# Optimization experiments

Measured on AMD Instinct MI355X. Metric: run time of the kernel, lower is better.

The kernel has to match this reference:

```python
import jax, jax.numpy as jnp
import numpy as np

N_NODES = 100000
N_EDGES = 1600000
D = 128  # feat_input_size_node == embed_inside_size == feat_target_size


def gcn_layer(x, W, b, row, col, ew, n_nodes):
    """PyG GCNConv with scalar edge_weight, add_self_loops=True, normalize=True.
    x: [N, Fin], W: [Fout, Fin], b: [Fout], row/col: [E], ew: [E].
    Messages flow row -> col (source_to_target)."""
    h = x @ W.T  # [N, Fout]
    # degree includes self-loop weight 1.0 per node
    deg = jax.ops.segment_sum(ew, col, num_segments=n_nodes) + 1.0  # [N]
    dinv = jnp.where(deg > 0, jax.lax.rsqrt(deg), 0.0)  # [N]
    norm = dinv[row] * ew * dinv[col]  # [E]
    msgs = norm[:, None] * h[row]  # [E, Fout] -- gather
    agg = jax.ops.segment_sum(msgs, col, num_segments=n_nodes)  # scatter-add
    agg = agg + (dinv * dinv)[:, None] * h  # self-loop contribution (weight 1)
    return agg + b


def setup_inputs() -> dict:
    key = jax.random.key(0)
    k1, k2, k3, k4, k5, k6, k7 = jax.random.split(key, 7)
    edge_tuples = jax.random.randint(k1, (2, N_EDGES), 0, N_NODES, dtype=jnp.int64) if jax.config.jax_enable_x64 else jax.random.randint(k1, (2, N_EDGES), 0, N_NODES).astype(jnp.int32)
    edge_feats = jax.random.uniform(k2, (N_EDGES, 1), dtype=jnp.float32)
    node_feats = jax.random.normal(k3, (N_NODES, D), dtype=jnp.float32)
    s1 = 1.0 / np.sqrt(D)
    W1 = jax.random.uniform(k4, (D, D), minval=-s1, maxval=s1, dtype=jnp.float32)
    b1 = jnp.zeros((D,), dtype=jnp.float32)
    W2 = jax.random.uniform(k5, (D, D), minval=-s1, maxval=s1, dtype=jnp.float32)
    b2 = jnp.zeros((D,), dtype=jnp.float32)
    return {"edge_tuples": edge_tuples, "edge_feats": edge_feats, "node_feats": node_feats,
            "W1": W1, "b1": b1, "W2": W2, "b2": b2}


def reference(edge_tuples, edge_feats, node_feats, W1, b1, W2, b2):
    row, col = edge_tuples[0], edge_tuples[1]
    ew = edge_feats.squeeze(-1)  # [E]
    n = node_feats.shape[0]
    h = gcn_layer(node_feats, W1, b1, row, col, ew, n)
    h = jnp.tanh(h)  # activate='tanh' between the two GCN layers
    out = gcn_layer(h, W2, b2, row, col, ew, n)
    # skip=Identity (Fin==Fout), doskip=1
    return out + node_feats
```

## Files before the change

### kernel.cpp

```cpp
#include <hip/hip_runtime.h>
#include <math.h>

#define D 128
#define EPB 4096
#define MAXNB 800

typedef unsigned long long ull;
typedef unsigned short ushort_t;
typedef __attribute__((ext_vector_type(8))) short bf16x8;
typedef __attribute__((ext_vector_type(4))) float f32x4;

__device__ __forceinline__ float bf_lo(unsigned u) { return __uint_as_float(u << 16); }
__device__ __forceinline__ float bf_hi(unsigned u) { return __uint_as_float(u & 0xffff0000u); }
__device__ __forceinline__ unsigned bpack(float a, float b) {
  unsigned ua = __float_as_uint(a), ub = __float_as_uint(b);
  ua += 0x7fff + ((ua >> 16) & 1);
  ub += 0x7fff + ((ub >> 16) & 1);
  return (ua >> 16) | (ub & 0xffff0000u);
}
__device__ __forceinline__ ushort_t bh16(float a) {
  unsigned ua = __float_as_uint(a);
  ua += 0x7fff + ((ua >> 16) & 1);
  return (ushort_t)(ua >> 16);
}

__global__ __launch_bounds__(256) void k_h1(const int* __restrict__ col, int E, int B1, int B1pad,
                                            int* __restrict__ gh, int NB,
                                            const float2* __restrict__ x2, unsigned* __restrict__ xb, int n64,
                                            const float* __restrict__ W1, const float* __restrict__ W2,
                                            ushort_t* __restrict__ Whi1, ushort_t* __restrict__ Wlo1,
                                            ushort_t* __restrict__ Whi2, ushort_t* __restrict__ Wlo2) {
  int b = blockIdx.x, t = threadIdx.x;
  if (b < B1) {
    __shared__ int h[MAXNB];
    for (int i = t; i < NB; i += 256) h[i] = 0;
    __syncthreads();
    int e0 = b * EPB, e1 = min(E, e0 + EPB);
    for (int e = e0 + t; e < e1; e += 256) atomicAdd(&h[col[e] >> 7], 1);
    __syncthreads();
    for (int i = t; i < NB; i += 256) gh[i * B1pad + b] = h[i];
    return;
  }
  int idx = (b - B1) * 256 + t;
  if (idx < n64) { float2 v = x2[idx]; xb[idx] = bpack(v.x, v.y); return; }
  int j = idx - n64;
  if (j >= 2 * D * D) return;
  const float* W = (j < D * D) ? W1 : W2;
  ushort_t* Hh = (j < D * D) ? Whi1 : Whi2;
  ushort_t* Hl = (j < D * D) ? Wlo1 : Wlo2;
  int k = j & (D * D - 1);
  float w = W[k];
  ushort_t hh = bh16(w);
  Hh[k] = hh;
  Hl[k] = bh16(w - __uint_as_float((unsigned)hh << 16));
}

__global__ __launch_bounds__(512) void k_hscan(int* __restrict__ gh, int* __restrict__ binTotal,
                                               int B1, int B1pad) {
  __shared__ int wsum[8];
  int bin = blockIdx.x, t = threadIdx.x;
  int v = (t < B1) ? gh[bin * B1pad + t] : 0;
  int lane = t & 63, wid = t >> 6;
  int x = v;
  #pragma unroll
  for (int d = 1; d < 64; d <<= 1) { int y = __shfl_up(x, d, 64); if (lane >= d) x += y; }
  if (lane == 63) wsum[wid] = x;
  __syncthreads();
  int woff = 0;
  for (int w = 0; w < wid; ++w) woff += wsum[w];
  if (t < B1) gh[bin * B1pad + t] = woff + x - v;
  if (t == 511) binTotal[bin] = woff + x;
}

__device__ __forceinline__ int block_excl_scan(int v, int t, int* wsum, int* total) {
  int lane = t & 63, wid = t >> 6;
  int x = v;
  #pragma unroll
  for (int d = 1; d < 64; d <<= 1) {
    int y = __shfl_up(x, d, 64);
    if (lane >= d) x += y;
  }
  if (lane == 63) wsum[wid] = x;
  __syncthreads();
  int woff = 0;
  for (int w = 0; w < wid; ++w) woff += wsum[w];
  if (total) { int tot = 0; for (int w = 0; w < 4; ++w) tot += wsum[w]; *total = tot; }
  return woff + x - v;
}

__global__ __launch_bounds__(256) void k_scatter(const int* __restrict__ row, const int* __restrict__ col,
                                                 const float* __restrict__ ew,
                                                 const int* __restrict__ gh, const int* __restrict__ binTotal,
                                                 int B1pad, int NB,
                                                 ull* __restrict__ a_e, int E) {
  __shared__ ull recs[EPB];
  __shared__ int hist[MAXNB];
  __shared__ int cur[MAXNB];
  __shared__ int wb[MAXNB];
  __shared__ int bbase[MAXNB];
  __shared__ int wsum[4];
  int b = blockIdx.x, t = threadIdx.x;
  for (int i = t; i < NB; i += 256) { hist[i] = 0; cur[i] = 0; }
  __syncthreads();
  int e0 = b * EPB;
  int cnt = min(E - e0, EPB);
  ull v[16];
  #pragma unroll
  for (int k = 0; k < 16; ++k) {
    int idx = t + k * 256;
    v[k] = 0;
    if (idx < cnt) {
      int e = e0 + idx;
      int c = col[e];
      unsigned q = __float2uint_rn(ew[e] * 32767.0f);
      if (q > 32767u) q = 32767u;
      unsigned hi = ((unsigned)c << 15) | q;
      v[k] = ((ull)hi << 32) | (unsigned)row[e];
      atomicAdd(&hist[hi >> 22], 1);
    }
  }
  __syncthreads();
  int base = t * 4;
  int bt[4]; int sb = 0;
  #pragma unroll
  for (int u = 0; u < 4; ++u) { bt[u] = (base + u < NB) ? binTotal[base + u] : 0; sb += bt[u]; }
  int exb = block_excl_scan(sb, t, wsum, nullptr);
  {
    int run = exb;
    #pragma unroll
    for (int u = 0; u < 4; ++u) { if (base + u < NB) bbase[base + u] = run; run += bt[u]; }
  }
  __syncthreads();
  int hv[4];
  #pragma unroll
  for (int u = 0; u < 4; ++u) hv[u] = (base + u < NB) ? hist[base + u] : 0;
  int s = hv[0] + hv[1] + hv[2] + hv[3];
  int excl = block_excl_scan(s, t, wsum, nullptr);
  int run = excl;
  #pragma unroll
  for (int u = 0; u < 4; ++u) {
    if (base + u < NB) {
      hist[base + u] = run;
      wb[base + u] = bbase[base + u] + gh[(base + u) * B1pad + b] - run;
    }
    run += hv[u];
  }
  __syncthreads();
  #pragma unroll
  for (int k = 0; k < 16; ++k) {
    if (t + k * 256 < cnt) {
      unsigned bkt = (unsigned)(v[k] >> 54);
      int idx = hist[bkt] + atomicAdd(&cur[bkt], 1);
      recs[idx] = v[k];
    }
  }
  __syncthreads();
  for (int i = t; i < cnt; i += 256) {
    ull r = recs[i];
    a_e[wb[(unsigned)(r >> 54)] + i] = r;
  }
}

__global__ __launch_bounds__(256) void k_bucket(const ull* __restrict__ a_e,
                                                const int* __restrict__ binTotal,
                                                int* __restrict__ offs, float* __restrict__ dinv,
                                                unsigned* __restrict__ sorted2, int N, int E, int NB) {
  __shared__ int hist[128];
  __shared__ float wdeg[128];
  __shared__ int pfx[128];
  __shared__ int cur[128];
  __shared__ int wred[4];
  __shared__ int s0sh;
  int bin = blockIdx.x, t = threadIdx.x;
  if (t < 128) { hist[t] = 0; wdeg[t] = 0.f; cur[t] = 0; }
  int part = 0;
  for (int j = t; j < NB; j += 256) if (j < bin) part += binTotal[j];
  #pragma unroll
  for (int d = 32; d >= 1; d >>= 1) part += __shfl_xor(part, d, 64);
  if ((t & 63) == 0) wred[t >> 6] = part;
  __syncthreads();
  if (t == 0) s0sh = wred[0] + wred[1] + wred[2] + wred[3];
  if (t == 0 && bin == 0) offs[N] = E;
  __syncthreads();
  int s0 = s0sh;
  int s1 = s0 + binTotal[bin];
  for (int i = s0 + t; i < s1; i += 256) {
    unsigned hi = (unsigned)(a_e[i] >> 32);
    int lc = (hi >> 15) & 127;
    atomicAdd(&hist[lc], 1);
    atomicAdd(&wdeg[lc], (float)(hi & 32767u) * (1.0f / 32767.0f));
  }
  __syncthreads();
  if (t == 0) { int run = 0; for (int i = 0; i < 128; ++i) { pfx[i] = run; run += hist[i]; } }
  __syncthreads();
  int c0 = bin << 7;
  if (t < 128 && c0 + t < N) {
    offs[c0 + t] = s0 + pfx[t];
    dinv[c0 + t] = rsqrtf(wdeg[t] + 1.0f);
  }
  for (int i = s0 + t; i < s1; i += 256) {
    ull v = a_e[i];
    unsigned hi = (unsigned)(v >> 32);
    int lc = (hi >> 15) & 127;
    int pos = s0 + pfx[lc] + atomicAdd(&cur[lc], 1);
    sorted2[pos] = ((unsigned)v << 15) | (hi & 32767u);
  }
}

__global__ __launch_bounds__(256) void k_agg(const unsigned* __restrict__ H2,
                                             const unsigned* __restrict__ elist,
                                             const int* __restrict__ offs, const float* __restrict__ dinv,
                                             unsigned* __restrict__ outb, int N) {
  int lane = threadIdx.x & 63;
  int c = blockIdx.x * 4 + (threadIdx.x >> 6);
  if (c >= N) return;
  int start = offs[c];
  int m = offs[c + 1] - start;
  int q = lane >> 4;
  int fi = lane & 15;
  float dv = dinv[c];
  float dcs = dv * (1.0f / 32767.0f);
  float a0 = 0.f, a1 = 0.f, a2 = 0.f, a3 = 0.f, a4 = 0.f, a5 = 0.f, a6 = 0.f, a7 = 0.f;
  for (int base = 0; base < m; base += 64) {
    int chunk = min(64, m - base);
    unsigned rec = (lane < chunk) ? elist[start + base + lane] : 0u;
    int iters = (chunk + 3) >> 2;
    int i = 0;
    for (; i + 4 <= iters; i += 4) {
      unsigned e0 = __shfl(rec, 4 * i + q, 64);
      unsigned e1 = __shfl(rec, 4 * i + 4 + q, 64);
      unsigned e2 = __shfl(rec, 4 * i + 8 + q, 64);
      unsigned e3 = __shfl(rec, 4 * i + 12 + q, 64);
      uint4 u0 = *(const uint4*)&H2[(size_t)(e0 >> 15) * 64 + fi * 4];
      uint4 u1 = *(const uint4*)&H2[(size_t)(e1 >> 15) * 64 + fi * 4];
      uint4 u2 = *(const uint4*)&H2[(size_t)(e2 >> 15) * 64 + fi * 4];
      uint4 u3 = *(const uint4*)&H2[(size_t)(e3 >> 15) * 64 + fi * 4];
      float w0 = (float)(e0 & 0x7fffu) * dinv[e0 >> 15] * dcs;
      float w1 = (float)(e1 & 0x7fffu) * dinv[e1 >> 15] * dcs;
      float w2 = (float)(e2 & 0x7fffu) * dinv[e2 >> 15] * dcs;
      float w3 = (float)(e3 & 0x7fffu) * dinv[e3 >> 15] * dcs;
      a0 += w0 * bf_lo(u0.x); a1 += w0 * bf_hi(u0.x);
      a2 += w0 * bf_lo(u0.y); a3 += w0 * bf_hi(u0.y);
      a4 += w0 * bf_lo(u0.z); a5 += w0 * bf_hi(u0.z);
      a6 += w0 * bf_lo(u0.w); a7 += w0 * bf_hi(u0.w);
      a0 += w1 * bf_lo(u1.x); a1 += w1 * bf_hi(u1.x);
      a2 += w1 * bf_lo(u1.y); a3 += w1 * bf_hi(u1.y);
      a4 += w1 * bf_lo(u1.z); a5 += w1 * bf_hi(u1.z);
      a6 += w1 * bf_lo(u1.w); a7 += w1 * bf_hi(u1.w);
      a0 += w2 * bf_lo(u2.x); a1 += w2 * bf_hi(u2.x);
      a2 += w2 * bf_lo(u2.y); a3 += w2 * bf_hi(u2.y);
      a4 += w2 * bf_lo(u2.z); a5 += w2 * bf_hi(u2.z);
      a6 += w2 * bf_lo(u2.w); a7 += w2 * bf_hi(u2.w);
      a0 += w3 * bf_lo(u3.x); a1 += w3 * bf_hi(u3.x);
      a2 += w3 * bf_lo(u3.y); a3 += w3 * bf_hi(u3.y);
      a4 += w3 * bf_lo(u3.z); a5 += w3 * bf_hi(u3.z);
      a6 += w3 * bf_lo(u3.w); a7 += w3 * bf_hi(u3.w);
    }
    for (; i < iters; ++i) {
      unsigned e0 = __shfl(rec, 4 * i + q, 64);
      float w0 = (float)(e0 & 0x7fffu) * dinv[e0 >> 15] * dcs;
      uint4 u0 = *(const uint4*)&H2[(size_t)(e0 >> 15) * 64 + fi * 4];
      a0 += w0 * bf_lo(u0.x); a1 += w0 * bf_hi(u0.x);
      a2 += w0 * bf_lo(u0.y); a3 += w0 * bf_hi(u0.y);
      a4 += w0 * bf_lo(u0.z); a5 += w0 * bf_hi(u0.z);
      a6 += w0 * bf_lo(u0.w); a7 += w0 * bf_hi(u0.w);
    }
  }
  a0 += __shfl_xor(a0, 16, 64); a0 += __shfl_xor(a0, 32, 64);
  a1 += __shfl_xor(a1, 16, 64); a1 += __shfl_xor(a1, 32, 64);
  a2 += __shfl_xor(a2, 16, 64); a2 += __shfl_xor(a2, 32, 64);
  a3 += __shfl_xor(a3, 16, 64); a3 += __shfl_xor(a3, 32, 64);
  a4 += __shfl_xor(a4, 16, 64); a4 += __shfl_xor(a4, 32, 64);
  a5 += __shfl_xor(a5, 16, 64); a5 += __shfl_xor(a5, 32, 64);
  a6 += __shfl_xor(a6, 16, 64); a6 += __shfl_xor(a6, 32, 64);
  a7 += __shfl_xor(a7, 16, 64); a7 += __shfl_xor(a7, 32, 64);
  if (q == 0) {
    float sw = dv * dv;
    uint4 us = *(const uint4*)&H2[(size_t)c * 64 + fi * 4];
    a0 += sw * bf_lo(us.x); a1 += sw * bf_hi(us.x);
    a2 += sw * bf_lo(us.y); a3 += sw * bf_hi(us.y);
    a4 += sw * bf_lo(us.z); a5 += sw * bf_hi(us.z);
    a6 += sw * bf_lo(us.w); a7 += sw * bf_hi(us.w);
    uint4 o;
    o.x = bpack(a0, a1); o.y = bpack(a2, a3); o.z = bpack(a4, a5); o.w = bpack(a6, a7);
    *(uint4*)&outb[(size_t)c * 64 + fi * 4] = o;
  }
}

template<int TANH, int SKIP>
__global__ __launch_bounds__(256) void k_mgemm(const ushort_t* __restrict__ S,
                                               const ushort_t* __restrict__ Whi,
                                               const ushort_t* __restrict__ Wlo,
                                               const float* __restrict__ bias,
                                               const ushort_t* __restrict__ skipb,
                                               void* __restrict__ outv, int n) {
  int wave = threadIdx.x >> 6, lane = threadIdx.x & 63;
  int cl = lane & 15;
  int kg = lane >> 4;
  int cb0 = wave * 2;

  bf16x8 bh[2][4], bl[2][4];
  float bv[2];
  #pragma unroll
  for (int c = 0; c < 2; ++c) {
    int col = (cb0 + c) * 16 + cl;
    const ushort_t* wh = Whi + (size_t)col * D + kg * 8;
    const ushort_t* wl = Wlo + (size_t)col * D + kg * 8;
    #pragma unroll
    for (int kt = 0; kt < 4; ++kt) {
      bh[c][kt] = *(const bf16x8*)(wh + kt * 32);
      bl[c][kt] = *(const bf16x8*)(wl + kt * 32);
    }
    bv[c] = bias[col];
  }

  int ntiles = (n + 15) >> 4;
  for (int t = blockIdx.x; t < ntiles; t += gridDim.x) {
    int arow = t * 16 + cl; if (arow >= n) arow = n - 1;
    const ushort_t* srow = S + (size_t)arow * D + kg * 8;
    bf16x8 a[4];
    #pragma unroll
    for (int kt = 0; kt < 4; ++kt) a[kt] = *(const bf16x8*)(srow + kt * 32);
    #pragma unroll
    for (int c = 0; c < 2; ++c) {
      f32x4 acc = {0.f, 0.f, 0.f, 0.f};
      #pragma unroll
      for (int kt = 0; kt < 4; ++kt)
        acc = __builtin_amdgcn_mfma_f32_16x16x32_bf16(a[kt], bh[c][kt], acc, 0, 0, 0);
      #pragma unroll
      for (int kt = 0; kt < 4; ++kt)
        acc = __builtin_amdgcn_mfma_f32_16x16x32_bf16(a[kt], bl[c][kt], acc, 0, 0, 0);
      int col = (cb0 + c) * 16 + cl;
      #pragma unroll
      for (int i = 0; i < 4; ++i) {
        int r = t * 16 + kg * 4 + i;
        if (r < n) {
          float o = acc[i] + bv[c];
          if (TANH) {
            o = tanhf(o);
            ((ushort_t*)outv)[(size_t)r * D + col] = bh16(o);
          } else {
            if (SKIP) o += __uint_as_float((unsigned)skipb[(size_t)r * D + col] << 16);
            ((float*)outv)[(size_t)r * D + col] = o;
          }
        }
      }
    }
  }
}

extern "C" void kernel_launch(void* const* d_in, const int* in_sizes, int n_in,
                              void* d_out, int out_size, void* d_ws, size_t ws_size,
                              hipStream_t stream) {
  const int*   et = (const int*)d_in[0];
  const float* ef = (const float*)d_in[1];
  const float* x  = (const float*)d_in[2];
  const float* W1 = (const float*)d_in[3];
  const float* b1 = (const float*)d_in[4];
  const float* W2 = (const float*)d_in[5];
  const float* b2 = (const float*)d_in[6];

  int E = in_sizes[1];
  int N = in_sizes[2] / D;
  const int* row = et;
  const int* col = et + E;

  int NB = (N + 127) >> 7;
  int B1 = (E + EPB - 1) / EPB;
  int B1pad = (B1 + 7) & ~7;

  char* p = (char*)d_ws;
  auto alloc = [&](size_t bytes) { char* q = p; p += (bytes + 255) & ~(size_t)255; return q; };
  int*      gh       = (int*)     alloc((size_t)NB * B1pad * 4);
  int*      binTotal = (int*)     alloc((size_t)NB * 4);
  ull*      a_e      = (ull*)     alloc((size_t)E * 8);
  unsigned* elist    = (unsigned*)alloc((size_t)E * 4);
  int*      offs     = (int*)     alloc((size_t)(N + 1) * 4);
  float*    dinv     = (float*)   alloc((size_t)N * 4);
  unsigned* xb       = (unsigned*)alloc((size_t)N * 64 * 4);
  unsigned* s2b      = (unsigned*)alloc((size_t)N * 64 * 4);
  ushort_t* whi1 = (ushort_t*)alloc(D * D * 2);
  ushort_t* wlo1 = (ushort_t*)alloc(D * D * 2);
  ushort_t* whi2 = (ushort_t*)alloc(D * D * 2);
  ushort_t* wlo2 = (ushort_t*)alloc(D * D * 2);
  unsigned* s1b = (unsigned*)d_out;
  unsigned* a1b = s1b + (size_t)N * 64;

  int prepBlocks = (N * 64 + 2 * D * D + 255) / 256;
  k_h1<<<B1 + prepBlocks, 256, 0, stream>>>(col, E, B1, B1pad, gh, NB,
                                            (const float2*)x, xb, N * 64,
                                            W1, W2, whi1, wlo1, whi2, wlo2);
  k_hscan<<<NB, 512, 0, stream>>>(gh, binTotal, B1, B1pad);
  k_scatter<<<B1, 256, 0, stream>>>(row, col, ef, gh, binTotal, B1pad, NB, a_e, E);
  k_bucket<<<NB, 256, 0, stream>>>(a_e, binTotal, offs, dinv, elist, N, E, NB);

  int ab = (N + 3) / 4;
  int gb = 1024;
  k_agg<<<ab, 256, 0, stream>>>(xb, elist, offs, dinv, s1b, N);
  k_mgemm<1, 0><<<gb, 256, 0, stream>>>((const ushort_t*)s1b, whi1, wlo1, b1, nullptr, a1b, N);
  k_agg<<<ab, 256, 0, stream>>>(a1b, elist, offs, dinv, s2b, N);
  k_mgemm<0, 1><<<gb, 256, 0, stream>>>((const ushort_t*)s2b, whi2, wlo2, b2,
                                        (const ushort_t*)xb, d_out, N);
}
```

Baseline: 240.0 us.

## Halve scatter block size and stage bucket sort through LDS

```diff
diff --git a/kernel.cpp b/kernel.cpp
--- a/kernel.cpp
+++ b/kernel.cpp
@@ -2,8 +2,9 @@
 #include <math.h>
 
 #define D 128
-#define EPB 4096
+#define EPB 2048
 #define MAXNB 800
+#define BCAP 3072
 
 typedef unsigned long long ull;
 typedef unsigned short ushort_t;
@@ -55,9 +56,9 @@
   Hl[k] = bh16(w - __uint_as_float((unsigned)hh << 16));
 }
 
-__global__ __launch_bounds__(512) void k_hscan(int* __restrict__ gh, int* __restrict__ binTotal,
-                                               int B1, int B1pad) {
-  __shared__ int wsum[8];
+__global__ __launch_bounds__(1024) void k_hscan(int* __restrict__ gh, int* __restrict__ binTotal,
+                                                int B1, int B1pad) {
+  __shared__ int wsum[16];
   int bin = blockIdx.x, t = threadIdx.x;
   int v = (t < B1) ? gh[bin * B1pad + t] : 0;
   int lane = t & 63, wid = t >> 6;
@@ -69,7 +70,7 @@
   int woff = 0;
   for (int w = 0; w < wid; ++w) woff += wsum[w];
   if (t < B1) gh[bin * B1pad + t] = woff + x - v;
-  if (t == 511) binTotal[bin] = woff + x;
+  if (t == 1023) binTotal[bin] = woff + x;
 }
 
 __device__ __forceinline__ int block_excl_scan(int v, int t, int* wsum, int* total) {
@@ -104,9 +105,9 @@
   __syncthreads();
   int e0 = b * EPB;
   int cnt = min(E - e0, EPB);
-  ull v[16];
-  #pragma unroll
-  for (int k = 0; k < 16; ++k) {
+  ull v[EPB / 256];
+  #pragma unroll
+  for (int k = 0; k < EPB / 256; ++k) {
     int idx = t + k * 256;
     v[k] = 0;
     if (idx < cnt) {
@@ -147,7 +148,7 @@
   }
   __syncthreads();
   #pragma unroll
-  for (int k = 0; k < 16; ++k) {
+  for (int k = 0; k < EPB / 256; ++k) {
     if (t + k * 256 < cnt) {
       unsigned bkt = (unsigned)(v[k] >> 54);
       int idx = hist[bkt] + atomicAdd(&cur[bkt], 1);
@@ -165,6 +166,8 @@
                                                 const int* __restrict__ binTotal,
                                                 int* __restrict__ offs, float* __restrict__ dinv,
                                                 unsigned* __restrict__ sorted2, int N, int E, int NB) {
+  __shared__ ull recLds[BCAP];
+  __shared__ unsigned sortLds[BCAP];
   __shared__ int hist[128];
   __shared__ float wdeg[128];
   __shared__ int pfx[128];
@@ -183,9 +186,14 @@
   if (t == 0 && bin == 0) offs[N] = E;
   __syncthreads();
   int s0 = s0sh;
-  int s1 = s0 + binTotal[bin];
-  for (int i = s0 + t; i < s1; i += 256) {
-    unsigned hi = (unsigned)(a_e[i] >> 32);
+  int cnt = binTotal[bin];
+  int fits = (cnt <= BCAP);
+  if (fits) {
+    for (int i = t; i < cnt; i += 256) recLds[i] = a_e[s0 + i];
+    __syncthreads();
+  }
+  for (int i = t; i < cnt; i += 256) {
+    unsigned hi = (unsigned)((fits ? recLds[i] : a_e[s0 + i]) >> 32);
     int lc = (hi >> 15) & 127;
     atomicAdd(&hist[lc], 1);
     atomicAdd(&wdeg[lc], (float)(hi & 32767u) * (1.0f / 32767.0f));
@@ -198,12 +206,17 @@
     offs[c0 + t] = s0 + pfx[t];
     dinv[c0 + t] = rsqrtf(wdeg[t] + 1.0f);
   }
-  for (int i = s0 + t; i < s1; i += 256) {
-    ull v = a_e[i];
+  for (int i = t; i < cnt; i += 256) {
+    ull v = fits ? recLds[i] : a_e[s0 + i];
     unsigned hi = (unsigned)(v >> 32);
     int lc = (hi >> 15) & 127;
-    int pos = s0 + pfx[lc] + atomicAdd(&cur[lc], 1);
-    sorted2[pos] = ((unsigned)v << 15) | (hi & 32767u);
+    int pos = pfx[lc] + atomicAdd(&cur[lc], 1);
+    unsigned sv = ((unsigned)v << 15) | (hi & 32767u);
+    if (fits) sortLds[pos] = sv; else sorted2[s0 + pos] = sv;
+  }
+  if (fits) {
+    __syncthreads();
+    for (int i = t; i < cnt; i += 256) sorted2[s0 + i] = sortLds[i];
   }
 }
 
@@ -390,7 +403,7 @@
   k_h1<<<B1 + prepBlocks, 256, 0, stream>>>(col, E, B1, B1pad, gh, NB,
                                             (const float2*)x, xb, N * 64,
                                             W1, W2, whi1, wlo1, whi2, wlo2);
-  k_hscan<<<NB, 512, 0, stream>>>(gh, binTotal, B1, B1pad);
+  k_hscan<<<NB, 1024, 0, stream>>>(gh, binTotal, B1, B1pad);
   k_scatter<<<B1, 256, 0, stream>>>(row, col, ef, gh, binTotal, B1pad, NB, a_e, E);
   k_bucket<<<NB, 256, 0, stream>>>(a_e, binTotal, offs, dinv, elist, N, E, NB);
 
```

Result: slower. 245.8 us (+2.4%).

## Fuse neighbor aggregation with the MFMA GEMM through an LDS row tile

Applied to the files above, without the earlier changes.

```diff
diff --git a/kernel.cpp b/kernel.cpp
--- a/kernel.cpp
+++ b/kernel.cpp
@@ -207,142 +207,132 @@
   }
 }
 
-__global__ __launch_bounds__(256) void k_agg(const unsigned* __restrict__ H2,
-                                             const unsigned* __restrict__ elist,
-                                             const int* __restrict__ offs, const float* __restrict__ dinv,
-                                             unsigned* __restrict__ outb, int N) {
-  int lane = threadIdx.x & 63;
-  int c = blockIdx.x * 4 + (threadIdx.x >> 6);
-  if (c >= N) return;
-  int start = offs[c];
-  int m = offs[c + 1] - start;
-  int q = lane >> 4;
-  int fi = lane & 15;
-  float dv = dinv[c];
-  float dcs = dv * (1.0f / 32767.0f);
-  float a0 = 0.f, a1 = 0.f, a2 = 0.f, a3 = 0.f, a4 = 0.f, a5 = 0.f, a6 = 0.f, a7 = 0.f;
-  for (int base = 0; base < m; base += 64) {
-    int chunk = min(64, m - base);
-    unsigned rec = (lane < chunk) ? elist[start + base + lane] : 0u;
-    int iters = (chunk + 3) >> 2;
-    int i = 0;
-    for (; i + 4 <= iters; i += 4) {
-      unsigned e0 = __shfl(rec, 4 * i + q, 64);
-      unsigned e1 = __shfl(rec, 4 * i + 4 + q, 64);
-      unsigned e2 = __shfl(rec, 4 * i + 8 + q, 64);
-      unsigned e3 = __shfl(rec, 4 * i + 12 + q, 64);
-      uint4 u0 = *(const uint4*)&H2[(size_t)(e0 >> 15) * 64 + fi * 4];
-      uint4 u1 = *(const uint4*)&H2[(size_t)(e1 >> 15) * 64 + fi * 4];
-      uint4 u2 = *(const uint4*)&H2[(size_t)(e2 >> 15) * 64 + fi * 4];
-      uint4 u3 = *(const uint4*)&H2[(size_t)(e3 >> 15) * 64 + fi * 4];
-      float w0 = (float)(e0 & 0x7fffu) * dinv[e0 >> 15] * dcs;
-      float w1 = (float)(e1 & 0x7fffu) * dinv[e1 >> 15] * dcs;
-      float w2 = (float)(e2 & 0x7fffu) * dinv[e2 >> 15] * dcs;
-      float w3 = (float)(e3 & 0x7fffu) * dinv[e3 >> 15] * dcs;
-      a0 += w0 * bf_lo(u0.x); a1 += w0 * bf_hi(u0.x);
-      a2 += w0 * bf_lo(u0.y); a3 += w0 * bf_hi(u0.y);
-      a4 += w0 * bf_lo(u0.z); a5 += w0 * bf_hi(u0.z);
-      a6 += w0 * bf_lo(u0.w); a7 += w0 * bf_hi(u0.w);
-      a0 += w1 * bf_lo(u1.x); a1 += w1 * bf_hi(u1.x);
-      a2 += w1 * bf_lo(u1.y); a3 += w1 * bf_hi(u1.y);
-      a4 += w1 * bf_lo(u1.z); a5 += w1 * bf_hi(u1.z);
-      a6 += w1 * bf_lo(u1.w); a7 += w1 * bf_hi(u1.w);
-      a0 += w2 * bf_lo(u2.x); a1 += w2 * bf_hi(u2.x);
-      a2 += w2 * bf_lo(u2.y); a3 += w2 * bf_hi(u2.y);
-      a4 += w2 * bf_lo(u2.z); a5 += w2 * bf_hi(u2.z);
-      a6 += w2 * bf_lo(u2.w); a7 += w2 * bf_hi(u2.w);
-      a0 += w3 * bf_lo(u3.x); a1 += w3 * bf_hi(u3.x);
-      a2 += w3 * bf_lo(u3.y); a3 += w3 * bf_hi(u3.y);
-      a4 += w3 * bf_lo(u3.z); a5 += w3 * bf_hi(u3.z);
-      a6 += w3 * bf_lo(u3.w); a7 += w3 * bf_hi(u3.w);
-    }
-    for (; i < iters; ++i) {
-      unsigned e0 = __shfl(rec, 4 * i + q, 64);
-      float w0 = (float)(e0 & 0x7fffu) * dinv[e0 >> 15] * dcs;
-      uint4 u0 = *(const uint4*)&H2[(size_t)(e0 >> 15) * 64 + fi * 4];
-      a0 += w0 * bf_lo(u0.x); a1 += w0 * bf_hi(u0.x);
-      a2 += w0 * bf_lo(u0.y); a3 += w0 * bf_hi(u0.y);
-      a4 += w0 * bf_lo(u0.z); a5 += w0 * bf_hi(u0.z);
-      a6 += w0 * bf_lo(u0.w); a7 += w0 * bf_hi(u0.w);
-    }
-  }
-  a0 += __shfl_xor(a0, 16, 64); a0 += __shfl_xor(a0, 32, 64);
-  a1 += __shfl_xor(a1, 16, 64); a1 += __shfl_xor(a1, 32, 64);
-  a2 += __shfl_xor(a2, 16, 64); a2 += __shfl_xor(a2, 32, 64);
-  a3 += __shfl_xor(a3, 16, 64); a3 += __shfl_xor(a3, 32, 64);
-  a4 += __shfl_xor(a4, 16, 64); a4 += __shfl_xor(a4, 32, 64);
-  a5 += __shfl_xor(a5, 16, 64); a5 += __shfl_xor(a5, 32, 64);
-  a6 += __shfl_xor(a6, 16, 64); a6 += __shfl_xor(a6, 32, 64);
-  a7 += __shfl_xor(a7, 16, 64); a7 += __shfl_xor(a7, 32, 64);
-  if (q == 0) {
-    float sw = dv * dv;
-    uint4 us = *(const uint4*)&H2[(size_t)c * 64 + fi * 4];
-    a0 += sw * bf_lo(us.x); a1 += sw * bf_hi(us.x);
-    a2 += sw * bf_lo(us.y); a3 += sw * bf_hi(us.y);
-    a4 += sw * bf_lo(us.z); a5 += sw * bf_hi(us.z);
-    a6 += sw * bf_lo(us.w); a7 += sw * bf_hi(us.w);
-    uint4 o;
-    o.x = bpack(a0, a1); o.y = bpack(a2, a3); o.z = bpack(a4, a5); o.w = bpack(a6, a7);
-    *(uint4*)&outb[(size_t)c * 64 + fi * 4] = o;
-  }
-}
-
 template<int TANH, int SKIP>
-__global__ __launch_bounds__(256) void k_mgemm(const ushort_t* __restrict__ S,
+__global__ __launch_bounds__(256) void k_aggmm(const unsigned* __restrict__ H2,
+                                               const unsigned* __restrict__ elist,
+                                               const int* __restrict__ offs, const float* __restrict__ dinv,
                                                const ushort_t* __restrict__ Whi,
                                                const ushort_t* __restrict__ Wlo,
                                                const float* __restrict__ bias,
                                                const ushort_t* __restrict__ skipb,
-                                               void* __restrict__ outv, int n) {
-  int wave = threadIdx.x >> 6, lane = threadIdx.x & 63;
-  int cl = lane & 15;
-  int kg = lane >> 4;
+                                               void* __restrict__ outv, int N) {
+  __shared__ ushort_t sRow[16][136];
+  int t = threadIdx.x;
+  int wave = t >> 6, lane = t & 63;
+  int q = lane >> 4;
+  int fi = lane & 15;
+  int blk = blockIdx.x;
+
+  for (int sub = 0; sub < 4; ++sub) {
+    int row = wave * 4 + sub;
+    int c = blk * 16 + row;
+    if (c < N) {
+      int start = offs[c];
+      int m = offs[c + 1] - start;
+      float dv = dinv[c];
+      float dcs = dv * (1.0f / 32767.0f);
+      float a0 = 0.f, a1 = 0.f, a2 = 0.f, a3 = 0.f, a4 = 0.f, a5 = 0.f, a6 = 0.f, a7 = 0.f;
+      for (int base = 0; base < m; base += 64) {
+        int chunk = min(64, m - base);
+        unsigned rec = (lane < chunk) ? elist[start + base + lane] : 0u;
+        int iters = (chunk + 3) >> 2;
+        int i = 0;
+        for (; i + 4 <= iters; i += 4) {
+          unsigned e0 = __shfl(rec, 4 * i + q, 64);
+          unsigned e1 = __shfl(rec, 4 * i + 4 + q, 64);
+          unsigned e2 = __shfl(rec, 4 * i + 8 + q, 64);
+          unsigned e3 = __shfl(rec, 4 * i + 12 + q, 64);
+          uint4 u0 = *(const uint4*)&H2[(size_t)(e0 >> 15) * 64 + fi * 4];
+          uint4 u1 = *(const uint4*)&H2[(size_t)(e1 >> 15) * 64 + fi * 4];
+          uint4 u2 = *(const uint4*)&H2[(size_t)(e2 >> 15) * 64 + fi * 4];
+          uint4 u3 = *(const uint4*)&H2[(size_t)(e3 >> 15) * 64 + fi * 4];
+          float w0 = (float)(e0 & 0x7fffu) * dinv[e0 >> 15] * dcs;
+          float w1 = (float)(e1 & 0x7fffu) * dinv[e1 >> 15] * dcs;
+          float w2 = (float)(e2 & 0x7fffu) * dinv[e2 >> 15] * dcs;
+          float w3 = (float)(e3 & 0x7fffu) * dinv[e3 >> 15] * dcs;
+          a0 += w0 * bf_lo(u0.x); a1 += w0 * bf_hi(u0.x);
+          a2 += w0 * bf_lo(u0.y); a3 += w0 * bf_hi(u0.y);
+          a4 += w0 * bf_lo(u0.z); a5 += w0 * bf_hi(u0.z);
+          a6 += w0 * bf_lo(u0.w); a7 += w0 * bf_hi(u0.w);
+          a0 += w1 * bf_lo(u1.x); a1 += w1 * bf_hi(u1.x);
+          a2 += w1 * bf_lo(u1.y); a3 += w1 * bf_hi(u1.y);
+          a4 += w1 * bf_lo(u1.z); a5 += w1 * bf_hi(u1.z);
+          a6 += w1 * bf_lo(u1.w); a7 += w1 * bf_hi(u1.w);
+          a0 += w2 * bf_lo(u2.x); a1 += w2 * bf_hi(u2.x);
+          a2 += w2 * bf_lo(u2.y); a3 += w2 * bf_hi(u2.y);
+          a4 += w2 * bf_lo(u2.z); a5 += w2 * bf_hi(u2.z);
+          a6 += w2 * bf_lo(u2.w); a7 += w2 * bf_hi(u2.w);
+          a0 += w3 * bf_lo(u3.x); a1 += w3 * bf_hi(u3.x);
+          a2 += w3 * bf_lo(u3.y); a3 += w3 * bf_hi(u3.y);
+          a4 += w3 * bf_lo(u3.z); a5 += w3 * bf_hi(u3.z);
+          a6 += w3 * bf_lo(u3.w); a7 += w3 * bf_hi(u3.w);
+        }
+        for (; i < iters; ++i) {
+          unsigned e0 = __shfl(rec, 4 * i + q, 64);
+          float w0 = (float)(e0 & 0x7fffu) * dinv[e0 >> 15] * dcs;
+          uint4 u0 = *(const uint4*)&H2[(size_t)(e0 >> 15) * 64 + fi * 4];
+          a0 += w0 * bf_lo(u0.x); a1 += w0 * bf_hi(u0.x);
+          a2 += w0 * bf_lo(u0.y); a3 += w0 * bf_hi(u0.y);
+          a4 += w0 * bf_lo(u0.z); a5 += w0 * bf_hi(u0.z);
+          a6 += w0 * bf_lo(u0.w); a7 += w0 * bf_hi(u0.w);
+        }
+      }
+      a0 += __shfl_xor(a0, 16, 64); a0 += __shfl_xor(a0, 32, 64);
+      a1 += __shfl_xor(a1, 16, 64); a1 += __shfl_xor(a1, 32, 64);
+      a2 += __shfl_xor(a2, 16, 64); a2 += __shfl_xor(a2, 32, 64);
+      a3 += __shfl_xor(a3, 16, 64); a3 += __shfl_xor(a3, 32, 64);
+      a4 += __shfl_xor(a4, 16, 64); a4 += __shfl_xor(a4, 32, 64);
+      a5 += __shfl_xor(a5, 16, 64); a5 += __shfl_xor(a5, 32, 64);
+      a6 += __shfl_xor(a6, 16, 64); a6 += __shfl_xor(a6, 32, 64);
+      a7 += __shfl_xor(a7, 16, 64); a7 += __shfl_xor(a7, 32, 64);
+      if (q == 0) {
+        float sw = dv * dv;
+        uint4 us = *(const uint4*)&H2[(size_t)c * 64 + fi * 4];
+        a0 += sw * bf_lo(us.x); a1 += sw * bf_hi(us.x);
+        a2 += sw * bf_lo(us.y); a3 += sw * bf_hi(us.y);
+        a4 += sw * bf_lo(us.z); a5 += sw * bf_hi(us.z);
+        a6 += sw * bf_lo(us.w); a7 += sw * bf_hi(us.w);
+        uint4 o;
+        o.x = bpack(a0, a1); o.y = bpack(a2, a3); o.z = bpack(a4, a5); o.w = bpack(a6, a7);
+        *(uint4*)&sRow[row][fi * 8] = o;
+      }
+    } else if (q == 0) {
+      uint4 z = make_uint4(0, 0, 0, 0);
+      *(uint4*)&sRow[row][fi * 8] = z;
+    }
+  }
+  __syncthreads();
+
+  int cl = fi;
+  int kg = q;
   int cb0 = wave * 2;
-
-  bf16x8 bh[2][4], bl[2][4];
-  float bv[2];
-  #pragma unroll
-  for (int c = 0; c < 2; ++c) {
-    int col = (cb0 + c) * 16 + cl;
-    const ushort_t* wh = Whi + (size_t)col * D + kg * 8;
-    const ushort_t* wl = Wlo + (size_t)col * D + kg * 8;
+  bf16x8 a[4];
+  #pragma unroll
+  for (int kt = 0; kt < 4; ++kt) a[kt] = *(const bf16x8*)&sRow[cl][kg * 8 + kt * 32];
+  #pragma unroll
+  for (int cc = 0; cc < 2; ++cc) {
+    int colj = (cb0 + cc) * 16 + cl;
+    const ushort_t* wh = Whi + (size_t)colj * D + kg * 8;
+    const ushort_t* wl = Wlo + (size_t)colj * D + kg * 8;
+    f32x4 acc = {0.f, 0.f, 0.f, 0.f};
     #pragma unroll
-    for (int kt = 0; kt < 4; ++kt) {
-      bh[c][kt] = *(const bf16x8*)(wh + kt * 32);
-      bl[c][kt] = *(const bf16x8*)(wl + kt * 32);
-    }
-    bv[c] = bias[col];
-  }
-
-  int ntiles = (n + 15) >> 4;
-  for (int t = blockIdx.x; t < ntiles; t += gridDim.x) {
-    int arow = t * 16 + cl; if (arow >= n) arow = n - 1;
-    const ushort_t* srow = S + (size_t)arow * D + kg * 8;
-    bf16x8 a[4];
+    for (int kt = 0; kt < 4; ++kt)
+      acc = __builtin_amdgcn_mfma_f32_16x16x32_bf16(a[kt], *(const bf16x8*)(wh + kt * 32), acc, 0, 0, 0);
     #pragma unroll
-    for (int kt = 0; kt < 4; ++kt) a[kt] = *(const bf16x8*)(srow + kt * 32);
+    for (int kt = 0; kt < 4; ++kt)
+      acc = __builtin_amdgcn_mfma_f32_16x16x32_bf16(a[kt], *(const bf16x8*)(wl + kt * 32), acc, 0, 0, 0);
+    float bv = bias[colj];
     #pragma unroll
-    for (int c = 0; c < 2; ++c) {
-      f32x4 acc = {0.f, 0.f, 0.f, 0.f};
-      #pragma unroll
-      for (int kt = 0; kt < 4; ++kt)
-        acc = __builtin_amdgcn_mfma_f32_16x16x32_bf16(a[kt], bh[c][kt], acc, 0, 0, 0);
-      #pragma unroll
-      for (int kt = 0; kt < 4; ++kt)
-        acc = __builtin_amdgcn_mfma_f32_16x16x32_bf16(a[kt], bl[c][kt], acc, 0, 0, 0);
-      int col = (cb0 + c) * 16 + cl;
-      #pragma unroll
-      for (int i = 0; i < 4; ++i) {
-        int r = t * 16 + kg * 4 + i;
-        if (r < n) {
-          float o = acc[i] + bv[c];
-          if (TANH) {
-            o = tanhf(o);
-            ((ushort_t*)outv)[(size_t)r * D + col] = bh16(o);
-          } else {
-            if (SKIP) o += __uint_as_float((unsigned)skipb[(size_t)r * D + col] << 16);
-            ((float*)outv)[(size_t)r * D + col] = o;
-          }
+    for (int i = 0; i < 4; ++i) {
+      int r = blk * 16 + kg * 4 + i;
+      if (r < N) {
+        float o = acc[i] + bv;
+        if (TANH) {
+          o = tanhf(o);
+          ((ushort_t*)outv)[(size_t)r * D + colj] = bh16(o);
+        } else {
+          if (SKIP) o += __uint_as_float((unsigned)skipb[(size_t)r * D + colj] << 16);
+          ((float*)outv)[(size_t)r * D + colj] = o;
         }
       }
     }
@@ -378,13 +368,11 @@
   int*      offs     = (int*)     alloc((size_t)(N + 1) * 4);
   float*    dinv     = (float*)   alloc((size_t)N * 4);
   unsigned* xb       = (unsigned*)alloc((size_t)N * 64 * 4);
-  unsigned* s2b      = (unsigned*)alloc((size_t)N * 64 * 4);
+  unsigned* a1b      = (unsigned*)alloc((size_t)N * 64 * 4);
   ushort_t* whi1 = (ushort_t*)alloc(D * D * 2);
   ushort_t* wlo1 = (ushort_t*)alloc(D * D * 2);
   ushort_t* whi2 = (ushort_t*)alloc(D * D * 2);
   ushort_t* wlo2 = (ushort_t*)alloc(D * D * 2);
-  unsigned* s1b = (unsigned*)d_out;
-  unsigned* a1b = s1b + (size_t)N * 64;
 
   int prepBlocks = (N * 64 + 2 * D * D + 255) / 256;
   k_h1<<<B1 + prepBlocks, 256, 0, stream>>>(col, E, B1, B1pad, gh, NB,
@@ -394,11 +382,8 @@
   k_scatter<<<B1, 256, 0, stream>>>(row, col, ef, gh, binTotal, B1pad, NB, a_e, E);
   k_bucket<<<NB, 256, 0, stream>>>(a_e, binTotal, offs, dinv, elist, N, E, NB);
 
-  int ab = (N + 3) / 4;
-  int gb = 1024;
-  k_agg<<<ab, 256, 0, stream>>>(xb, elist, offs, dinv, s1b, N);
-  k_mgemm<1, 0><<<gb, 256, 0, stream>>>((const ushort_t*)s1b, whi1, wlo1, b1, nullptr, a1b, N);
-  k_agg<<<ab, 256, 0, stream>>>(a1b, elist, offs, dinv, s2b, N);
-  k_mgemm<0, 1><<<gb, 256, 0, stream>>>((const ushort_t*)s2b, whi2, wlo2, b2,
+  int fb = (N + 15) / 16;
+  k_aggmm<1, 0><<<fb, 256, 0, stream>>>(xb, elist, offs, dinv, whi1, wlo1, b1, nullptr, a1b, N);
+  k_aggmm<0, 1><<<fb, 256, 0, stream>>>(a1b, elist, offs, dinv, whi2, wlo2, b2,
                                         (const ushort_t*)xb, d_out, N);
 }
```

Result: slower. 258.2 us (+7.6%).
